# Optimization experiments

Measured on AMD Instinct MI355X. Metric: run time of the kernel, lower is better.

Reference implementation:

```python
import jax, jax.numpy as jnp
import numpy as np
from jax import lax

LPC_ORDER = 24  # M, even -> even-order branch
LOG_GAIN = False


def roots_to_poly(r):
    """Monic polynomial coefficients from roots r[..., n].

    Matches diffsptk RootsToPolynomial: c starts as [1,0,...,0] and for each
    root c[1:m+2] -= r_m * c[0:m+1], i.e. c <- c - r * shift_right(c).
    Returns coeffs of shape (..., n+1), descending powers, leading 1.
    """
    n = r.shape[-1]
    c0 = jnp.zeros(r.shape[:-1] + (n + 1,), dtype=r.dtype).at[..., 0].set(1.0)

    def step(c, rt):
        shifted = jnp.concatenate([jnp.zeros_like(c[..., :1]), c[..., :-1]], axis=-1)
        return c - rt[..., None] * shifted, None

    c, _ = lax.scan(step, c0, jnp.moveaxis(r, -1, 0))
    return c


def setup_inputs() -> dict:
    key = jax.random.key(0)
    # LSP frequencies in radians live in (0, pi); uniform [0,1) is in-range.
    w = jax.random.uniform(key, (512, 2048, LPC_ORDER + 1), dtype=jnp.float32)
    return {"w": w}


def reference(w):
    M = LPC_ORDER
    K = w[..., :1]
    if LOG_GAIN:
        K = jnp.exp(K)
    ang = w[..., 1:]                       # (..., M)
    z = jnp.exp(1j * ang.astype(jnp.complex64))
    p_r = z[..., 1::2]                     # (..., M//2)
    q_r = z[..., 0::2]                     # (..., M//2)
    # roots come in conjugate pairs -> real polynomials
    P = roots_to_poly(jnp.concatenate([p_r, jnp.conj(p_r)], axis=-1)).real  # (..., M+1)
    Q = roots_to_poly(jnp.concatenate([q_r, jnp.conj(q_r)], axis=-1)).real  # (..., M+1)
    # conv1d (cross-correlation) with kernel_p=[-1,1], kernel_q=[1,1], no padding (even M)
    p_c = P[..., 1:] - P[..., :-1]         # (..., M)
    q_c = Q[..., :-1] + Q[..., 1:]         # (..., M)
    a = 0.5 * (p_c + q_c)
    return jnp.concatenate([K, a], axis=-1)
```

## Files before the change

kernel.cpp:

```cpp
#include <hip/hip_runtime.h>


typedef float f4 __attribute__((ext_vector_type(4)));
typedef float f2 __attribute__((ext_vector_type(2)));

static constexpr int NC  = 25;
static constexpr int RPB = 256;
static constexpr int FPB = NC * RPB;
static constexpr int V4  = FPB / 4;
static constexpr int TAIL = V4 - 6 * RPB;

__global__ __launch_bounds__(256)
void lsp2lpc_kernel(const float* __restrict__ in, float* __restrict__ out) {
    __shared__ float lds[FPB];
    const int tid = threadIdx.x;
    const size_t base = (size_t)blockIdx.x * FPB;

    const f4* gin  = reinterpret_cast<const f4*>(in + base);
    f4*       lds4 = reinterpret_cast<f4*>(lds);
#pragma unroll
    for (int i = 0; i < 6; ++i)
        lds4[tid + i * RPB] = gin[tid + i * RPB];
    if (tid < TAIL)
        lds4[tid + 6 * RPB] = gin[tid + 6 * RPB];
    __syncthreads();

    const float* row = &lds[tid * NC];
    const float K = row[0];
    f2 t[12];
#pragma unroll
    for (int m = 0; m < 12; ++m) {
        const float cq = __cosf(row[1 + 2 * m]);
        const float cp = __cosf(row[2 + 2 * m]);
        t[m] = (f2){-2.f * cp, -2.f * cq};
    }

    f2 PQ[13];
#pragma unroll
    for (int k = 0; k < 13; ++k) PQ[k] = (f2){0.f, 0.f};
    PQ[0] = (f2){1.f, 1.f};

#pragma unroll
    for (int m = 0; m < 12; ++m) {
        const f2 tm = t[m];
        const int kmax = (2 * m + 2 < 12) ? (2 * m + 2) : 12;
#pragma unroll
        for (int k = 12; k >= 0; --k) {
            if (k > kmax) continue;
            const f2 c1 = (k >= 1) ? PQ[k - 1] : (f2){0.f, 0.f};
            const f2 c2 = (k >= 2) ? PQ[k - 2] : (f2){0.f, 0.f};
            PQ[k] = __builtin_elementwise_fma(tm, c1, PQ[k]) + c2;
        }
    }
    __syncthreads();

    float u[13], v[13];
#pragma unroll
    for (int k = 0; k < 13; ++k) {
        u[k] = PQ[k].x + PQ[k].y;
        v[k] = PQ[k].y - PQ[k].x;
    }
    float* orow = &lds[tid * NC];
    orow[0] = K;
#pragma unroll
    for (int k = 0; k < 24; ++k) {
        const int i0 = (k     <= 12) ? k       : 24 - k;
        const int i1 = (k + 1 <= 12) ? (k + 1) : 24 - (k + 1);
        orow[1 + k] = 0.5f * (u[i1] + v[i0]);
    }
    __syncthreads();

    f4* gout = reinterpret_cast<f4*>(out + base);
#pragma unroll
    for (int i = 0; i < 6; ++i)
        __builtin_nontemporal_store(lds4[tid + i * RPB], &gout[tid + i * RPB]);
    if (tid < TAIL)
        __builtin_nontemporal_store(lds4[tid + 6 * RPB], &gout[tid + 6 * RPB]);
}

extern "C" void kernel_launch(void* const* d_in, const int* in_sizes, int n_in,
                              void* d_out, int out_size, void* d_ws, size_t ws_size,
                              hipStream_t stream) {
    const float* in  = (const float*)d_in[0];
    float*       out = (float*)d_out;
    const int nrows   = in_sizes[0] / NC;
    const int nblocks = nrows / RPB;
    lsp2lpc_kernel<<<nblocks, RPB, 0, stream>>>(in, out);
}
```

Baseline: 37.59 us.

## Process four tiles per block with register prefetch of next tile

Each block now loops over four row tiles. While it computes the current tile out of LDS, it loads the next tile from global memory into registers, then stages that tile into LDS after storing the current output. The goal is to overlap global load latency with compute and to amortize block launch. The trade-off is fewer blocks, higher register pressure and extra barriers, which can lower occupancy.

```diff
diff --git a/kernel.cpp b/kernel.cpp
--- a/kernel.cpp
+++ b/kernel.cpp
@@ -4,78 +4,105 @@
 typedef float f4 __attribute__((ext_vector_type(4)));
 typedef float f2 __attribute__((ext_vector_type(2)));
 
-static constexpr int NC  = 25;
-static constexpr int RPB = 256;
-static constexpr int FPB = NC * RPB;
-static constexpr int V4  = FPB / 4;
+static constexpr int NC   = 25;
+static constexpr int RPB  = 256;
+static constexpr int FPB  = NC * RPB;
+static constexpr int V4   = FPB / 4;
 static constexpr int TAIL = V4 - 6 * RPB;
+static constexpr int TPB_TILES = 4;
+
+__device__ __forceinline__ void load_tile_regs(const float* __restrict__ in,
+                                               int tile, int tid, f4* pf) {
+    const f4* gin = reinterpret_cast<const f4*>(in + (size_t)tile * FPB);
+#pragma unroll
+    for (int i = 0; i < 6; ++i)
+        pf[i] = gin[tid + i * RPB];
+    pf[6] = (tid < TAIL) ? gin[tid + 6 * RPB] : (f4){0.f, 0.f, 0.f, 0.f};
+}
+
+__device__ __forceinline__ void write_regs_lds(f4* lds4, int tid, const f4* pf) {
+#pragma unroll
+    for (int i = 0; i < 6; ++i)
+        lds4[tid + i * RPB] = pf[i];
+    if (tid < TAIL)
+        lds4[tid + 6 * RPB] = pf[6];
+}
 
 __global__ __launch_bounds__(256)
 void lsp2lpc_kernel(const float* __restrict__ in, float* __restrict__ out) {
     __shared__ float lds[FPB];
     const int tid = threadIdx.x;
-    const size_t base = (size_t)blockIdx.x * FPB;
+    f4* lds4 = reinterpret_cast<f4*>(lds);
+    const int tile0 = blockIdx.x * TPB_TILES;
 
-    const f4* gin  = reinterpret_cast<const f4*>(in + base);
-    f4*       lds4 = reinterpret_cast<f4*>(lds);
-#pragma unroll
-    for (int i = 0; i < 6; ++i)
-        lds4[tid + i * RPB] = gin[tid + i * RPB];
-    if (tid < TAIL)
-        lds4[tid + 6 * RPB] = gin[tid + 6 * RPB];
+    f4 pf[7];
+    load_tile_regs(in, tile0, tid, pf);
+    write_regs_lds(lds4, tid, pf);
     __syncthreads();
 
-    const float* row = &lds[tid * NC];
-    const float K = row[0];
-    f2 t[12];
+    for (int t = 0; t < TPB_TILES; ++t) {
+        const int tile = tile0 + t;
+
+        if (t + 1 < TPB_TILES)
+            load_tile_regs(in, tile + 1, tid, pf);
+
+        const float* row = &lds[tid * NC];
+        const float K = row[0];
+        f2 tcoef[12];
 #pragma unroll
-    for (int m = 0; m < 12; ++m) {
-        const float cq = __cosf(row[1 + 2 * m]);
-        const float cp = __cosf(row[2 + 2 * m]);
-        t[m] = (f2){-2.f * cp, -2.f * cq};
-    }
+        for (int m = 0; m < 12; ++m) {
+            const float cq = __cosf(row[1 + 2 * m]);
+            const float cp = __cosf(row[2 + 2 * m]);
+            tcoef[m] = (f2){-2.f * cp, -2.f * cq};
+        }
 
-    f2 PQ[13];
+        f2 PQ[13];
 #pragma unroll
-    for (int k = 0; k < 13; ++k) PQ[k] = (f2){0.f, 0.f};
-    PQ[0] = (f2){1.f, 1.f};
+        for (int k = 0; k < 13; ++k) PQ[k] = (f2){0.f, 0.f};
+        PQ[0] = (f2){1.f, 1.f};
 
 #pragma unroll
-    for (int m = 0; m < 12; ++m) {
-        const f2 tm = t[m];
-        const int kmax = (2 * m + 2 < 12) ? (2 * m + 2) : 12;
+        for (int m = 0; m < 12; ++m) {
+            const f2 tm = tcoef[m];
+            const int kmax = (2 * m + 2 < 12) ? (2 * m + 2) : 12;
 #pragma unroll
-        for (int k = 12; k >= 0; --k) {
-            if (k > kmax) continue;
-            const f2 c1 = (k >= 1) ? PQ[k - 1] : (f2){0.f, 0.f};
-            const f2 c2 = (k >= 2) ? PQ[k - 2] : (f2){0.f, 0.f};
-            PQ[k] = __builtin_elementwise_fma(tm, c1, PQ[k]) + c2;
+            for (int k = 12; k >= 0; --k) {
+                if (k > kmax) continue;
+                const f2 c1 = (k >= 1) ? PQ[k - 1] : (f2){0.f, 0.f};
+                const f2 c2 = (k >= 2) ? PQ[k - 2] : (f2){0.f, 0.f};
+                PQ[k] = __builtin_elementwise_fma(tm, c1, PQ[k]) + c2;
+            }
+        }
+
+        float u[13], v[13];
+#pragma unroll
+        for (int k = 0; k < 13; ++k) {
+            u[k] = PQ[k].x + PQ[k].y;
+            v[k] = PQ[k].y - PQ[k].x;
+        }
+        float* orow = &lds[tid * NC];
+        orow[0] = K;
+#pragma unroll
+        for (int k = 0; k < 24; ++k) {
+            const int i0 = (k     <= 12) ? k       : 24 - k;
+            const int i1 = (k + 1 <= 12) ? (k + 1) : 24 - (k + 1);
+            orow[1 + k] = 0.5f * (u[i1] + v[i0]);
+        }
+        __syncthreads();
+
+        f4* gout = reinterpret_cast<f4*>(out + (size_t)tile * FPB);
+#pragma unroll
+        for (int i = 0; i < 6; ++i)
+            __builtin_nontemporal_store(lds4[tid + i * RPB], &gout[tid + i * RPB]);
+        if (tid < TAIL)
+            __builtin_nontemporal_store(lds4[tid + 6 * RPB], &gout[tid + 6 * RPB]);
+
+        if (t + 1 < TPB_TILES) {
+            __syncthreads();
+            write_regs_lds(lds4, tid, pf);
+            __syncthreads();
         }
     }
-    __syncthreads();
-
-    float u[13], v[13];
-#pragma unroll
-    for (int k = 0; k < 13; ++k) {
-        u[k] = PQ[k].x + PQ[k].y;
-        v[k] = PQ[k].y - PQ[k].x;
-    }
-    float* orow = &lds[tid * NC];
-    orow[0] = K;
-#pragma unroll
-    for (int k = 0; k < 24; ++k) {
-        const int i0 = (k     <= 12) ? k       : 24 - k;
-        const int i1 = (k + 1 <= 12) ? (k + 1) : 24 - (k + 1);
-        orow[1 + k] = 0.5f * (u[i1] + v[i0]);
-    }
-    __syncthreads();
-
-    f4* gout = reinterpret_cast<f4*>(out + base);
-#pragma unroll
-    for (int i = 0; i < 6; ++i)
-        __builtin_nontemporal_store(lds4[tid + i * RPB], &gout[tid + i * RPB]);
-    if (tid < TAIL)
-        __builtin_nontemporal_store(lds4[tid + 6 * RPB], &gout[tid + 6 * RPB]);
 }
 
 extern "C" void kernel_launch(void* const* d_in, const int* in_sizes, int n_in,
@@ -84,6 +111,7 @@
     const float* in  = (const float*)d_in[0];
     float*       out = (float*)d_out;
     const int nrows   = in_sizes[0] / NC;
-    const int nblocks = nrows / RPB;
+    const int ntiles  = nrows / RPB;
+    const int nblocks = ntiles / TPB_TILES;
     lsp2lpc_kernel<<<nblocks, RPB, 0, stream>>>(in, out);
 }
```

After: 37.34 us. Within noise of the previous version (-0.7%).
